# Kernel tuning notes

Hardware: AMD Instinct MI355X
Metric: run time of the kernel (lower is better)

The kernel has to match this reference:

```python
import jax, jax.numpy as jnp
import numpy as np

N = 50000
E = 800000
GENE = 256
H = 128
BN_EPS = 1e-5


def _lin(key, fan_in, fan_out):
    k1, k2 = jax.random.split(key)
    w = jax.random.normal(k1, (fan_in, fan_out), jnp.float32) * (1.0 / np.sqrt(fan_in))
    b = jax.random.normal(k2, (fan_out,), jnp.float32) * 0.01
    return w, b


def setup_inputs() -> dict:
    key = jax.random.key(0)
    ks = jax.random.split(key, 32)
    inp = {}
    inp['x'] = jax.random.normal(ks[0], (N, GENE), jnp.float32)
    inp['edge_index'] = jax.random.randint(ks[1], (2, E), 0, N, jnp.int32)
    dims = [(GENE, H), (H, 2 * H), (2 * H, H), (H, H // 2)]
    ki = 2
    for i, (din, dout) in enumerate(dims, start=1):
        wa, ba = _lin(ks[ki], din, dout); ki += 1
        wb, bb = _lin(ks[ki], dout, dout); ki += 1
        inp[f'w{i}a'], inp[f'b{i}a'] = wa, ba
        inp[f'w{i}b'], inp[f'b{i}b'] = wb, bb
        inp[f'bn{i}_g'] = jnp.ones((dout,), jnp.float32)
        inp[f'bn{i}_b'] = jnp.zeros((dout,), jnp.float32)
        inp[f'bn{i}_m'] = jax.random.normal(ks[ki], (dout,), jnp.float32) * 0.1; ki += 1
        inp[f'bn{i}_v'] = jax.random.uniform(ks[ki], (dout,), jnp.float32, 0.5, 1.5); ki += 1
    wc, bc = _lin(ks[ki], H // 2, 2)
    inp['wc'], inp['bc'] = wc, bc
    return inp


def _gin_layer(h, src, dst, wa, ba, wb, bb, g, be, m, v):
    # GINConv (eps=0): z = x + sum_{j in N(i)} x_j, then 2-layer MLP
    agg = jax.ops.segment_sum(h[src], dst, num_segments=N)
    z = h + agg
    z = jax.nn.relu(z @ wa + ba) @ wb + bb
    # BatchNorm1d (eval: running stats) + ReLU
    z = (z - m) * jax.lax.rsqrt(v + BN_EPS) * g + be
    return jax.nn.relu(z)


def reference(x, edge_index,
              w1a, b1a, w1b, b1b, bn1_g, bn1_b, bn1_m, bn1_v,
              w2a, b2a, w2b, b2b, bn2_g, bn2_b, bn2_m, bn2_v,
              w3a, b3a, w3b, b3b, bn3_g, bn3_b, bn3_m, bn3_v,
              w4a, b4a, w4b, b4b, bn4_g, bn4_b, bn4_m, bn4_v,
              wc, bc):
    src, dst = edge_index[0], edge_index[1]
    h = _gin_layer(x, src, dst, w1a, b1a, w1b, b1b, bn1_g, bn1_b, bn1_m, bn1_v)
    h = _gin_layer(h, src, dst, w2a, b2a, w2b, b2b, bn2_g, bn2_b, bn2_m, bn2_v)
    h = _gin_layer(h, src, dst, w3a, b3a, w3b, b3b, bn3_g, bn3_b, bn3_m, bn3_v)
    h = _gin_layer(h, src, dst, w4a, b4a, w4b, b4b, bn4_g, bn4_b, bn4_m, bn4_v)
    return h @ wc + bc
```

## Files before the change

### kernel.cpp

```cpp
#include <hip/hip_runtime.h>

#define N_NODES 50000
#define N_EDGES 800000
#define BN_EPS 1e-5f
#define K_BUCK 196
#define PART_B 256
#define CHUNK 3125

typedef __attribute__((ext_vector_type(8))) short bshort8;
typedef __attribute__((ext_vector_type(4))) float f32x4;

__device__ inline float bf2f(unsigned int u16) {
    return __uint_as_float(u16 << 16);
}
__device__ inline unsigned short f2bf(float f) {
    unsigned int u = __float_as_uint(f);
    u = (u + 0x7FFFu + ((u >> 16) & 1u)) >> 16;
    return (unsigned short)u;
}


__device__ inline int block_exscan256(int v, int tid, int* total) {
    int lane = tid & 63;
    int wave = tid >> 6;
    int incl = v;
#pragma unroll
    for (int off = 1; off < 64; off <<= 1) {
        int t = __shfl_up(incl, off, 64);
        if (lane >= off) incl += t;
    }
    __shared__ int wsum[4];
    if (lane == 63) wsum[wave] = incl;
    __syncthreads();
    int w0 = wsum[0], w1 = wsum[1], w2 = wsum[2], w3 = wsum[3];
    __syncthreads();
    int wofs = (wave > 0 ? w0 : 0) + (wave > 1 ? w1 : 0) + (wave > 2 ? w2 : 0);
    *total = w0 + w1 + w2 + w3;
    return wofs + incl - v;
}

__global__ __launch_bounds__(256) void scan_reduce_kernel(const int* __restrict__ in,
                                                          int* __restrict__ bsum, int n) {
    int tid = threadIdx.x;
    int i = blockIdx.x * 256 + tid;
    int v = (i < n) ? in[i] : 0;
    int lane = tid & 63;
    int wave = tid >> 6;
#pragma unroll
    for (int off = 32; off > 0; off >>= 1) v += __shfl_down(v, off, 64);
    __shared__ int wsum[4];
    if (lane == 0) wsum[wave] = v;
    __syncthreads();
    if (tid == 0) bsum[blockIdx.x] = wsum[0] + wsum[1] + wsum[2] + wsum[3];
}

__global__ __launch_bounds__(256) void scan_bsum_kernel(int* __restrict__ bsum, int B) {
    int tid = threadIdx.x;
    int v = (tid < B) ? bsum[tid] : 0;
    int total;
    int excl = block_exscan256(v, tid, &total);
    if (tid < B) bsum[tid] = excl;
}

__global__ __launch_bounds__(256) void scan_apply_kernel(const int* __restrict__ in,
                                                         const int* __restrict__ bsum,
                                                         int* __restrict__ out, int n) {
    int tid = threadIdx.x;
    int i = blockIdx.x * 256 + tid;
    int v = (i < n) ? in[i] : 0;
    int total;
    int excl = block_exscan256(v, tid, &total);
    if (i < n) out[i] = bsum[blockIdx.x] + excl;
}


__global__ __launch_bounds__(256) void bucket_count_kernel(const int* __restrict__ dst,
                                                           int* __restrict__ deg,
                                                           int* __restrict__ cnt) {
    __shared__ int lcnt[K_BUCK];
    int tid = threadIdx.x;
    for (int i = tid; i < K_BUCK; i += 256) lcnt[i] = 0;
    __syncthreads();
    int start = blockIdx.x * CHUNK;
    for (int it = tid; it < CHUNK; it += 256) {
        int d = dst[start + it];
        atomicAdd(&lcnt[d >> 8], 1);
        atomicAdd(&deg[d], 1);
    }
    __syncthreads();
    for (int i = tid; i < K_BUCK; i += 256) cnt[i * PART_B + blockIdx.x] = lcnt[i];
}

__global__ __launch_bounds__(256) void partition_kernel(const int* __restrict__ src,
                                                        const int* __restrict__ dst,
                                                        const int* __restrict__ base,
                                                        uint2* __restrict__ P) {
    __shared__ int lofs[K_BUCK];
    int tid = threadIdx.x;
    for (int i = tid; i < K_BUCK; i += 256) lofs[i] = base[i * PART_B + blockIdx.x];
    __syncthreads();
    int start = blockIdx.x * CHUNK;
    for (int it = tid; it < CHUNK; it += 256) {
        int e = start + it;
        int d = dst[e], s = src[e];
        int p = atomicAdd(&lofs[d >> 8], 1);
        P[p] = make_uint2((unsigned)d, (unsigned)s);
    }
}

__global__ __launch_bounds__(256) void fine_scatter_kernel(const uint2* __restrict__ P,
                                                           const int* __restrict__ base,
                                                           const int* __restrict__ deg,
                                                           int* __restrict__ rowptr,
                                                           int* __restrict__ col) {
    __shared__ int wloc[256];
    int b = blockIdx.x;
    int tid = threadIdx.x;
    int nbase = b << 8;
    int nn = min(256, N_NODES - nbase);
    int d = (tid < nn) ? deg[nbase + tid] : 0;
    int total;
    int excl = block_exscan256(d, tid, &total);
    int start = base[b * PART_B];
    int rp = start + excl;
    if (tid < nn) {
        rowptr[nbase + tid] = rp;
        wloc[tid] = rp;
    }
    if (b == K_BUCK - 1 && tid == 0) rowptr[N_NODES] = N_EDGES;
    __syncthreads();
    int end = (b + 1 < K_BUCK) ? base[(b + 1) * PART_B] : N_EDGES;
    for (int e = start + tid; e < end; e += 256) {
        uint2 pr = P[e];
        int rank = atomicAdd(&wloc[pr.x - nbase], 1);
        col[rank] = (int)pr.y;
    }
}


struct WT8 {
    const float* src[8];
    unsigned short* dst[8];
    int K[8];
    int N[8];
};

__global__ __launch_bounds__(256) void wtconv_kernel(WT8 p) {
    int wi = blockIdx.y;
    int K = p.K[wi], N = p.N[wi];
    int idx = blockIdx.x * 256 + threadIdx.x;
    if (idx >= K * N) return;
    int logn = 31 - __clz(N);
    int n = idx & (N - 1);
    int k = idx >> logn;
    p.dst[wi][(size_t)n * K + k] = f2bf(p.src[wi][idx]);
}

__global__ __launch_bounds__(256) void wpconv_kernel(WT8 p) {
    int wi = blockIdx.y;
    int K = p.K[wi], N = p.N[wi];
    int idx = blockIdx.x * 256 + threadIdx.x;
    if (idx >= K * N) return;
    int S = K >> 5;
    int logs = 31 - __clz(S);
    int j = idx & 7;
    int l = (idx >> 3) & 63;
    int rest = idx >> 9;
    int s = rest & (S - 1);
    int t = rest >> logs;
    int k = s * 32 + ((l >> 4) << 3) + j;
    int n = t * 16 + (l & 15);
    p.dst[wi][idx] = f2bf(p.src[wi][(size_t)k * N + n]);
}


__device__ inline void acc8(uint4 v, float* a) {
    a[0] += bf2f(v.x & 0xFFFFu); a[1] += __uint_as_float(v.x & 0xFFFF0000u);
    a[2] += bf2f(v.y & 0xFFFFu); a[3] += __uint_as_float(v.y & 0xFFFF0000u);
    a[4] += bf2f(v.z & 0xFFFFu); a[5] += __uint_as_float(v.z & 0xFFFF0000u);
    a[6] += bf2f(v.w & 0xFFFFu); a[7] += __uint_as_float(v.w & 0xFFFF0000u);
}

template <int BM, int KIN, bool RELU>
__device__ inline void agg_head(const unsigned short* __restrict__ h,
                                const int* __restrict__ rowptr,
                                const int* __restrict__ col,
                                const float* __restrict__ bias,
                                unsigned short* __restrict__ As,
                                int row0, int M, int tid) {
    constexpr int LPN = KIN / 8;
    constexpr int GPS = 256 / LPN;
    constexpr int NSW = BM / GPS;
    constexpr int LDA = KIN + 8;
    const uint4* hv = (const uint4*)h;
    const int l = tid & (LPN - 1);
    const int g = tid / LPN;
#pragma unroll
    for (int sw = 0; sw < NSW; ++sw) {
        int r = sw * GPS + g;
        int node = row0 + r;
        uint4 o = make_uint4(0u, 0u, 0u, 0u);
        if (node < M) {
            float a[8] = {};
            uint4 vs = hv[(size_t)node * LPN + l];
            int s = rowptr[node], epos = rowptr[node + 1];
            int e = s;
            for (; e + 8 <= epos; e += 8) {
                int j0 = col[e],     j1 = col[e + 1], j2 = col[e + 2], j3 = col[e + 3];
                int j4 = col[e + 4], j5 = col[e + 5], j6 = col[e + 6], j7 = col[e + 7];
                uint4 v0 = hv[(size_t)j0 * LPN + l];
                uint4 v1 = hv[(size_t)j1 * LPN + l];
                uint4 v2 = hv[(size_t)j2 * LPN + l];
                uint4 v3 = hv[(size_t)j3 * LPN + l];
                uint4 v4 = hv[(size_t)j4 * LPN + l];
                uint4 v5 = hv[(size_t)j5 * LPN + l];
                uint4 v6 = hv[(size_t)j6 * LPN + l];
                uint4 v7 = hv[(size_t)j7 * LPN + l];
                acc8(v0, a); acc8(v1, a); acc8(v2, a); acc8(v3, a);
                acc8(v4, a); acc8(v5, a); acc8(v6, a); acc8(v7, a);
            }
            if (e + 4 <= epos) {
                int j0 = col[e], j1 = col[e + 1], j2 = col[e + 2], j3 = col[e + 3];
                uint4 v0 = hv[(size_t)j0 * LPN + l];
                uint4 v1 = hv[(size_t)j1 * LPN + l];
                uint4 v2 = hv[(size_t)j2 * LPN + l];
                uint4 v3 = hv[(size_t)j3 * LPN + l];
                acc8(v0, a); acc8(v1, a); acc8(v2, a); acc8(v3, a);
                e += 4;
            }
            if (e + 2 <= epos) {
                int j0 = col[e], j1 = col[e + 1];
                uint4 v0 = hv[(size_t)j0 * LPN + l];
                uint4 v1 = hv[(size_t)j1 * LPN + l];
                acc8(v0, a); acc8(v1, a);
                e += 2;
            }
            if (e < epos) acc8(hv[(size_t)col[e] * LPN + l], a);
            acc8(vs, a);
            if (RELU) {
                float4 b0 = *(const float4*)(bias + l * 8);
                float4 b1 = *(const float4*)(bias + l * 8 + 4);
                a[0] = fmaxf(a[0] + b0.x, 0.f); a[1] = fmaxf(a[1] + b0.y, 0.f);
                a[2] = fmaxf(a[2] + b0.z, 0.f); a[3] = fmaxf(a[3] + b0.w, 0.f);
                a[4] = fmaxf(a[4] + b1.x, 0.f); a[5] = fmaxf(a[5] + b1.y, 0.f);
                a[6] = fmaxf(a[6] + b1.z, 0.f); a[7] = fmaxf(a[7] + b1.w, 0.f);
            }
            o.x = (unsigned int)f2bf(a[0]) | ((unsigned int)f2bf(a[1]) << 16);
            o.y = (unsigned int)f2bf(a[2]) | ((unsigned int)f2bf(a[3]) << 16);
            o.z = (unsigned int)f2bf(a[4]) | ((unsigned int)f2bf(a[5]) << 16);
            o.w = (unsigned int)f2bf(a[6]) | ((unsigned int)f2bf(a[7]) << 16);
        }
        *(uint4*)(&As[r * LDA + l * 8]) = o;
    }
}


__device__ inline void epi_coeff(int mode, int c, const float* bias, const float* g,
                                 const float* be, const float* mu, const float* var,
                                 float* s, float* sh) {
    *s = 1.f; *sh = 0.f;
    if (mode == 0) {
        *sh = bias[c];
    } else if (mode == 1) {
        float t = g[c] * rsqrtf(var[c] + BN_EPS);
        *s = t;
        *sh = be[c] - mu[c] * t + bias[c] * t;
    }
}


template <int NT, bool F32A>
__global__ __launch_bounds__(256) void mfma_gemm2_kernel(
    const void* __restrict__ Ain, const unsigned short* __restrict__ Wt,
    unsigned short* __restrict__ C,
    int M, int K, int Nn, int mode, int gxblocks, int gy) {
    constexpr int BM = 128, BK = 64;
    constexpr int BN = NT * 16;
    constexpr int LDA = BK + 8;
    constexpr int LDB = BK + 8;
    constexpr int LDE = BN + 8;
    constexpr int NB_LD = (BN * BK / 8) / 256;
    __shared__ __align__(16) unsigned short smem[BM * LDA + BN * LDB];
    unsigned short* As = smem;
    unsigned short* Bs = smem + BM * LDA;
    unsigned short* Ep = smem;

    int id = blockIdx.x;
    int lo = id & 7;
    int t = id >> 3;
    int y = t % gy;
    int x = ((t / gy) << 3) | lo;
    if (x >= gxblocks) return;

    const int tid = threadIdx.x;
    const int wv = tid >> 6;
    const int ln = tid & 63;
    const int l15 = ln & 15;
    const int quad = ln >> 4;
    const int row0 = x * BM;
    const int col0 = y * BN;

    const unsigned short* A16 = (const unsigned short*)Ain;
    const float* A32 = (const float*)Ain;

    uint4 Ar[4], Br[NB_LD];

    auto loadA = [&](int k0) {
#pragma unroll
        for (int u = 0; u < 4; ++u) {
            int idx2 = tid + 256 * u;
            int r = idx2 >> 3, cg = (idx2 & 7) * 8;
            int gr = row0 + r;
            if (gr >= M) gr = M - 1;
            if (F32A) {
                float4 f0 = *(const float4*)(A32 + (size_t)gr * K + k0 + cg);
                float4 f1 = *(const float4*)(A32 + (size_t)gr * K + k0 + cg + 4);
                uint4 o;
                o.x = (unsigned)f2bf(f0.x) | ((unsigned)f2bf(f0.y) << 16);
                o.y = (unsigned)f2bf(f0.z) | ((unsigned)f2bf(f0.w) << 16);
                o.z = (unsigned)f2bf(f1.x) | ((unsigned)f2bf(f1.y) << 16);
                o.w = (unsigned)f2bf(f1.z) | ((unsigned)f2bf(f1.w) << 16);
                Ar[u] = o;
            } else {
                Ar[u] = *(const uint4*)(A16 + (size_t)gr * K + k0 + cg);
            }
        }
    };
    auto loadB = [&](int k0) {
#pragma unroll
        for (int u = 0; u < NB_LD; ++u) {
            int idx2 = tid + 256 * u;
            int r = idx2 >> 3, cg = (idx2 & 7) * 8;
            Br[u] = *(const uint4*)(Wt + (size_t)(col0 + r) * K + k0 + cg);
        }
    };
    auto stage = [&]() {
#pragma unroll
        for (int u = 0; u < 4; ++u) {
            int idx2 = tid + 256 * u;
            int r = idx2 >> 3, cg = (idx2 & 7) * 8;
            *(uint4*)(&As[r * LDA + cg]) = Ar[u];
        }
#pragma unroll
        for (int u = 0; u < NB_LD; ++u) {
            int idx2 = tid + 256 * u;
            int r = idx2 >> 3, cg = (idx2 & 7) * 8;
            *(uint4*)(&Bs[r * LDB + cg]) = Br[u];
        }
    };

    f32x4 acc[2][NT] = {};
    const int KT = K >> 6;
    loadA(0);
    loadB(0);
    for (int kt = 0; kt < KT; ++kt) {
        if (kt > 0) __syncthreads();
        stage();
        __syncthreads();
        if (kt + 1 < KT) {
            loadA((kt + 1) * 64);
            loadB((kt + 1) * 64);
        }
#pragma unroll
        for (int kh = 0; kh < 2; ++kh) {
            bshort8 af[2];
#pragma unroll
            for (int mt = 0; mt < 2; ++mt)
                af[mt] = *(const bshort8*)(&As[(wv * 32 + mt * 16 + l15) * LDA + kh * 32 + quad * 8]);
#pragma unroll
            for (int nt = 0; nt < NT; ++nt) {
                bshort8 bf = *(const bshort8*)(&Bs[(nt * 16 + l15) * LDB + kh * 32 + quad * 8]);
                acc[0][nt] = __builtin_amdgcn_mfma_f32_16x16x32_bf16(af[0], bf, acc[0][nt], 0, 0, 0);
                acc[1][nt] = __builtin_amdgcn_mfma_f32_16x16x32_bf16(af[1], bf, acc[1][nt], 0, 0, 0);
            }
        }
    }

    __syncthreads();
#pragma unroll
    for (int nt = 0; nt < NT; ++nt) {
#pragma unroll
        for (int mt = 0; mt < 2; ++mt) {
            int rl = wv * 32 + mt * 16 + quad * 4;
#pragma unroll
            for (int r = 0; r < 4; ++r) {
                float v = acc[mt][nt][r];
                if (mode != 2) v = fmaxf(v, 0.f);
                Ep[(rl + r) * LDE + nt * 16 + l15] = f2bf(v);
            }
        }
    }
    __syncthreads();
    constexpr int CGR = BN / 8;
    constexpr int NU = BM * CGR / 256;
#pragma unroll
    for (int u = 0; u < NU; ++u) {
        int idx2 = tid + 256 * u;
        int r = idx2 / CGR, cg = (idx2 % CGR) * 8;
        int grow = row0 + r;
        if (grow < M)
            *(uint4*)(C + (size_t)grow * Nn + col0 + cg) = *(const uint4*)(&Ep[r * LDE + cg]);
    }
}


template <int KIN, int DH>
__global__ __launch_bounds__(256, 4) void packed_gemm_kernel(
    const unsigned short* __restrict__ A, const unsigned short* __restrict__ Wp,
    int mode, const float* __restrict__ bias, const float* __restrict__ g,
    const float* __restrict__ be, const float* __restrict__ mu, const float* __restrict__ var,
    unsigned short* __restrict__ C, int M) {
    constexpr int BM = 64, BK = 64;
    constexpr int LDA = BK + 8;
    constexpr int LDE = DH + 8;
    constexpr int NT = DH / 64;
    constexpr int KT = KIN / 64;
    constexpr int S = KIN / 32;
    __shared__ __align__(16) unsigned short smem[BM * LDE];
    unsigned short* As = smem;
    unsigned short* Ep = smem;

    const int tid = threadIdx.x;
    const int wv = tid >> 6;
    const int ln = tid & 63;
    const int l15 = ln & 15;
    const int quad = ln >> 4;
    const int tb = wv * NT;
    const int ch = wv * (DH / 4);
    const int row0 = blockIdx.x * BM;

    uint4 Ar[2];
    auto loadA = [&](int k0) {
#pragma unroll
        for (int u = 0; u < 2; ++u) {
            int idx2 = tid + 256 * u;
            int r = idx2 >> 3, cg = (idx2 & 7) * 8;
            int gr = row0 + r;
            if (gr >= M) gr = M - 1;
            Ar[u] = *(const uint4*)(A + (size_t)gr * KIN + k0 + cg);
        }
    };
    auto stageA = [&]() {
#pragma unroll
        for (int u = 0; u < 2; ++u) {
            int idx2 = tid + 256 * u;
            int r = idx2 >> 3, cg = (idx2 & 7) * 8;
            *(uint4*)(&As[r * LDA + cg]) = Ar[u];
        }
    };
    auto loadB = [&](int s, bshort8* d) {
#pragma unroll
        for (int nt = 0; nt < NT; ++nt)
            d[nt] = *(const bshort8*)(Wp + ((size_t)((tb + nt) * S + s) * 64 + ln) * 8);
    };

    f32x4 acc[4][NT] = {};
    bshort8 bf[NT], bnx[NT];
    loadA(0);
    loadB(0, bf);
    for (int kt = 0; kt < KT; ++kt) {
        if (kt > 0) __syncthreads();
        stageA();
        __syncthreads();
        if (kt + 1 < KT) loadA((kt + 1) * 64);
#pragma unroll
        for (int kh = 0; kh < 2; ++kh) {
            int st = kt * 2 + kh;
            if (st + 1 < S) loadB(st + 1, bnx);
            bshort8 af[4];
#pragma unroll
            for (int mt = 0; mt < 4; ++mt)
                af[mt] = *(const bshort8*)(&As[(mt * 16 + l15) * LDA + kh * 32 + quad * 8]);
#pragma unroll
            for (int nt = 0; nt < NT; ++nt)
#pragma unroll
                for (int mt = 0; mt < 4; ++mt)
                    acc[mt][nt] = __builtin_amdgcn_mfma_f32_16x16x32_bf16(af[mt], bf[nt], acc[mt][nt], 0, 0, 0);
            if (st + 1 < S) {
#pragma unroll
                for (int nt = 0; nt < NT; ++nt) bf[nt] = bnx[nt];
            }
        }
    }
    __syncthreads();
#pragma unroll
    for (int nt = 0; nt < NT; ++nt) {
        int c = ch + nt * 16 + l15;
        float s, sh;
        epi_coeff(mode, c, bias, g, be, mu, var, &s, &sh);
#pragma unroll
        for (int mt = 0; mt < 4; ++mt) {
            int rl = mt * 16 + quad * 4;
#pragma unroll
            for (int r = 0; r < 4; ++r) {
                float v = acc[mt][nt][r] * s + sh;
                if (mode != 2) v = fmaxf(v, 0.f);
                Ep[(rl + r) * LDE + c] = f2bf(v);
            }
        }
    }
    __syncthreads();
    constexpr int CGR = DH / 8;
    constexpr int NU = BM * CGR / 256;
#pragma unroll
    for (int u = 0; u < NU; ++u) {
        int idx2 = tid + 256 * u;
        int r = idx2 / CGR, cg = (idx2 % CGR) * 8;
        int grow = row0 + r;
        if (grow < M)
            *(uint4*)(C + (size_t)grow * DH + cg) = *(const uint4*)(&Ep[r * LDE + cg]);
    }
}


template <int BM, int KIN, int DH, bool ARELU>
__global__ __launch_bounds__(256, 4) void agg_gemm_kernel(
    const unsigned short* __restrict__ h, const int* __restrict__ rowptr,
    const int* __restrict__ col, const float* __restrict__ abias,
    const unsigned short* __restrict__ Wp,
    int mode, const float* __restrict__ bias, const float* __restrict__ g,
    const float* __restrict__ be, const float* __restrict__ mu, const float* __restrict__ var,
    unsigned short* __restrict__ C, int M) {
    constexpr int MT = BM / 16;
    constexpr int LDA = KIN + 8;
    constexpr int LDE = DH + 8;
    constexpr int NT = DH / 64;
    constexpr int S = KIN / 32;
    constexpr int LMX = (LDA > LDE) ? LDA : LDE;
    __shared__ __align__(16) unsigned short smem[BM * LMX];
    unsigned short* As = smem;
    unsigned short* Ep = smem;

    const int tid = threadIdx.x;
    const int wv = tid >> 6;
    const int ln = tid & 63;
    const int l15 = ln & 15;
    const int quad = ln >> 4;
    const int tb = wv * NT;
    const int ch = wv * (DH / 4);
    const int row0 = blockIdx.x * BM;

    auto loadB = [&](int s, bshort8* d) {
#pragma unroll
        for (int nt = 0; nt < NT; ++nt)
            d[nt] = *(const bshort8*)(Wp + ((size_t)((tb + nt) * S + s) * 64 + ln) * 8);
    };

    bshort8 bf[NT], bnx[NT];
    loadB(0, bf);
    agg_head<BM, KIN, ARELU>(h, rowptr, col, abias, As, row0, M, tid);
    __syncthreads();

    f32x4 acc[MT][NT] = {};
#pragma unroll
    for (int ks = 0; ks < S; ++ks) {
        if (ks + 1 < S) loadB(ks + 1, bnx);
        bshort8 af[MT];
#pragma unroll
        for (int mt = 0; mt < MT; ++mt)
            af[mt] = *(const bshort8*)(&As[(mt * 16 + l15) * LDA + (ks >> 1) * 64 + (ks & 1) * 32 + quad * 8]);
#pragma unroll
        for (int nt = 0; nt < NT; ++nt)
#pragma unroll
            for (int mt = 0; mt < MT; ++mt)
                acc[mt][nt] = __builtin_amdgcn_mfma_f32_16x16x32_bf16(af[mt], bf[nt], acc[mt][nt], 0, 0, 0);
        if (ks + 1 < S) {
#pragma unroll
            for (int nt = 0; nt < NT; ++nt) bf[nt] = bnx[nt];
        }
    }
    __syncthreads();
#pragma unroll
    for (int nt = 0; nt < NT; ++nt) {
        int c = ch + nt * 16 + l15;
        float s, sh;
        epi_coeff(mode, c, bias, g, be, mu, var, &s, &sh);
#pragma unroll
        for (int mt = 0; mt < MT; ++mt) {
            int rl = mt * 16 + quad * 4;
#pragma unroll
            for (int r = 0; r < 4; ++r) {
                float v = acc[mt][nt][r] * s + sh;
                if (mode != 2) v = fmaxf(v, 0.f);
                Ep[(rl + r) * LDE + c] = f2bf(v);
            }
        }
    }
    __syncthreads();
    constexpr int CGR = DH / 8;
    constexpr int NU = BM * CGR / 256;
#pragma unroll
    for (int u = 0; u < NU; ++u) {
        int idx2 = tid + 256 * u;
        int r = idx2 / CGR, cg = (idx2 % CGR) * 8;
        int grow = row0 + r;
        if (grow < M)
            *(uint4*)(C + (size_t)grow * DH + cg) = *(const uint4*)(&Ep[r * LDE + cg]);
    }
}


template <int BM, int KIN, int DH1, int DH2, bool ARELU>
__global__ __launch_bounds__(256, 4) void agg_mlp_kernel(
    const unsigned short* __restrict__ h, const int* __restrict__ rowptr,
    const int* __restrict__ col, const float* __restrict__ abias,
    const unsigned short* __restrict__ Wp1, const unsigned short* __restrict__ Wp2,
    int mode1, const float* __restrict__ b1, const float* __restrict__ g1,
    const float* __restrict__ be1, const float* __restrict__ mu1, const float* __restrict__ var1,
    int mode2, const float* __restrict__ b2, const float* __restrict__ g2,
    const float* __restrict__ be2, const float* __restrict__ mu2, const float* __restrict__ var2,
    unsigned short* __restrict__ C, int M) {
    constexpr int MT = BM / 16;
    constexpr int LDA = KIN + 8;
    constexpr int LT1 = DH1 + 8;
    constexpr int LDE = DH2 + 8;
    constexpr int NT1 = DH1 / 64;
    constexpr int NT2 = DH2 / 64;
    constexpr int S1 = KIN / 32;
    constexpr int S2 = DH1 / 32;
    constexpr int LM0 = (LDA > LT1) ? LDA : LT1;
    constexpr int LMX = (LM0 > LDE) ? LM0 : LDE;
    __shared__ __align__(16) unsigned short smem[BM * LMX];
    unsigned short* As = smem;
    unsigned short* T1 = smem;

    const int tid = threadIdx.x;
    const int wv = tid >> 6;
    const int ln = tid & 63;
    const int l15 = ln & 15;
    const int quad = ln >> 4;
    const int tb1 = wv * NT1;
    const int tb2 = wv * NT2;
    const int ch1 = wv * (DH1 / 4);
    const int ch2 = wv * (DH2 / 4);
    const int row0 = blockIdx.x * BM;

    auto loadB1 = [&](int s, bshort8* d) {
#pragma unroll
        for (int nt = 0; nt < NT1; ++nt)
            d[nt] = *(const bshort8*)(Wp1 + ((size_t)((tb1 + nt) * S1 + s) * 64 + ln) * 8);
    };
    auto loadB2 = [&](int s, bshort8* d) {
#pragma unroll
        for (int nt = 0; nt < NT2; ++nt)
            d[nt] = *(const bshort8*)(Wp2 + ((size_t)((tb2 + nt) * S2 + s) * 64 + ln) * 8);
    };

    bshort8 bf[NT1], bnx[NT1], bf2[NT2];
    loadB1(0, bf);
    agg_head<BM, KIN, ARELU>(h, rowptr, col, abias, As, row0, M, tid);
    __syncthreads();

    f32x4 acc1[MT][NT1] = {};
#pragma unroll
    for (int ks = 0; ks < S1; ++ks) {
        if (ks + 1 < S1) loadB1(ks + 1, bnx);
        bshort8 af[MT];
#pragma unroll
        for (int mt = 0; mt < MT; ++mt)
            af[mt] = *(const bshort8*)(&As[(mt * 16 + l15) * LDA + (ks >> 1) * 64 + (ks & 1) * 32 + quad * 8]);
#pragma unroll
        for (int nt = 0; nt < NT1; ++nt)
#pragma unroll
            for (int mt = 0; mt < MT; ++mt)
                acc1[mt][nt] = __builtin_amdgcn_mfma_f32_16x16x32_bf16(af[mt], bf[nt], acc1[mt][nt], 0, 0, 0);
        if (ks + 1 < S1) {
#pragma unroll
            for (int nt = 0; nt < NT1; ++nt) bf[nt] = bnx[nt];
        }
    }
    __syncthreads();
#pragma unroll
    for (int nt = 0; nt < NT1; ++nt) {
        int c = ch1 + nt * 16 + l15;
        float s, sh;
        epi_coeff(mode1, c, b1, g1, be1, mu1, var1, &s, &sh);
#pragma unroll
        for (int mt = 0; mt < MT; ++mt) {
            int rl = mt * 16 + quad * 4;
#pragma unroll
            for (int r = 0; r < 4; ++r) {
                float v = acc1[mt][nt][r] * s + sh;
                if (mode1 != 2) v = fmaxf(v, 0.f);
                T1[(rl + r) * LT1 + c] = f2bf(v);
            }
        }
    }
    loadB2(0, bf2);
    __syncthreads();

    f32x4 acc2[MT][NT2] = {};
    bshort8 bnx2[NT2];
#pragma unroll
    for (int ks = 0; ks < S2; ++ks) {
        if (ks + 1 < S2) loadB2(ks + 1, bnx2);
        bshort8 af[MT];
#pragma unroll
        for (int mt = 0; mt < MT; ++mt)
            af[mt] = *(const bshort8*)(&T1[(mt * 16 + l15) * LT1 + ks * 32 + quad * 8]);
#pragma unroll
        for (int nt = 0; nt < NT2; ++nt)
#pragma unroll
            for (int mt = 0; mt < MT; ++mt)
                acc2[mt][nt] = __builtin_amdgcn_mfma_f32_16x16x32_bf16(af[mt], bf2[nt], acc2[mt][nt], 0, 0, 0);
        if (ks + 1 < S2) {
#pragma unroll
            for (int nt = 0; nt < NT2; ++nt) bf2[nt] = bnx2[nt];
        }
    }
    __syncthreads();

    unsigned short* Ep = T1;
#pragma unroll
    for (int nt = 0; nt < NT2; ++nt) {
        int c = ch2 + nt * 16 + l15;
        float s, sh;
        epi_coeff(mode2, c, b2, g2, be2, mu2, var2, &s, &sh);
#pragma unroll
        for (int mt = 0; mt < MT; ++mt) {
            int rl = mt * 16 + quad * 4;
#pragma unroll
            for (int r = 0; r < 4; ++r) {
                float v = acc2[mt][nt][r] * s + sh;
                if (mode2 != 2) v = fmaxf(v, 0.f);
                Ep[(rl + r) * LDE + c] = f2bf(v);
            }
        }
    }
    __syncthreads();
    constexpr int CGR = DH2 / 8;
    constexpr int NU = BM * CGR / 256;
#pragma unroll
    for (int u = 0; u < NU; ++u) {
        int idx2 = tid + 256 * u;
        int r = idx2 / CGR, cg = (idx2 % CGR) * 8;
        int grow = row0 + r;
        if (grow < M)
            *(uint4*)(C + (size_t)grow * DH2 + cg) = *(const uint4*)(&Ep[r * LDE + cg]);
    }
}


__global__ __launch_bounds__(256, 4) void agg_cls_kernel(
    const unsigned short* __restrict__ h, const int* __restrict__ rowptr,
    const int* __restrict__ col, const float* __restrict__ abias,
    const unsigned short* __restrict__ Wp,
    const float* __restrict__ bias, const float* __restrict__ g,
    const float* __restrict__ be, const float* __restrict__ mu, const float* __restrict__ var,
    const float* __restrict__ wcls, const float* __restrict__ bcls,
    float* __restrict__ outp, int M) {
    constexpr int BM = 64, KIN = 64, DH = 64;
    constexpr int LDA = KIN + 8;
    constexpr int LDE = DH + 8;
    constexpr int NT = 1;
    constexpr int S = KIN / 32;
    __shared__ __align__(16) unsigned short smem[BM * LDA];
    unsigned short* As = smem;
    unsigned short* Ep = smem;

    const int tid = threadIdx.x;
    const int wv = tid >> 6;
    const int ln = tid & 63;
    const int l15 = ln & 15;
    const int quad = ln >> 4;
    const int tb = wv;
    const int ch = wv * 16;
    const int row0 = blockIdx.x * BM;

    auto loadB = [&](int s, bshort8* d) {
        d[0] = *(const bshort8*)(Wp + ((size_t)(tb * S + s) * 64 + ln) * 8);
    };

    bshort8 bf[NT], bnx[NT];
    loadB(0, bf);
    agg_head<BM, KIN, true>(h, rowptr, col, abias, As, row0, M, tid);
    __syncthreads();

    f32x4 acc[4][NT] = {};
#pragma unroll
    for (int ks = 0; ks < S; ++ks) {
        if (ks + 1 < S) loadB(ks + 1, bnx);
        bshort8 af[4];
#pragma unroll
        for (int mt = 0; mt < 4; ++mt)
            af[mt] = *(const bshort8*)(&As[(mt * 16 + l15) * LDA + ks * 32 + quad * 8]);
#pragma unroll
        for (int mt = 0; mt < 4; ++mt)
            acc[mt][0] = __builtin_amdgcn_mfma_f32_16x16x32_bf16(af[mt], bf[0], acc[mt][0], 0, 0, 0);
        if (ks + 1 < S) bf[0] = bnx[0];
    }
    __syncthreads();
    {
        int c = ch + l15;
        float s, sh;
        epi_coeff(1, c, bias, g, be, mu, var, &s, &sh);
#pragma unroll
        for (int mt = 0; mt < 4; ++mt) {
            int rl = mt * 16 + quad * 4;
#pragma unroll
            for (int r = 0; r < 4; ++r) {
                float v = fmaxf(acc[mt][0][r] * s + sh, 0.f);
                Ep[(rl + r) * LDE + c] = f2bf(v);
            }
        }
    }
    __syncthreads();
    if (tid < 128) {
        int r = tid >> 1, j = tid & 1;
        int grow = row0 + r;
        if (grow < M) {
            float s = 0.f;
#pragma unroll 8
            for (int k = 0; k < 64; ++k)
                s += bf2f(Ep[r * LDE + k]) * wcls[k * 2 + j];
            outp[(size_t)grow * 2 + j] = s + bcls[j];
        }
    }
}


extern "C" void kernel_launch(void* const* d_in, const int* in_sizes, int n_in,
                              void* d_out, int out_size, void* d_ws, size_t ws_size,
                              hipStream_t stream) {
    const float* x = (const float*)d_in[0];
    const int* ei = (const int*)d_in[1];
    const int* src = ei;
    const int* dst = ei + N_EDGES;
    const float* w[4][2];
    const float* b[4][2];
    const float* bng[4];
    const float* bnb[4];
    const float* bnm[4];
    const float* bnv[4];
    int idx = 2;
    for (int i = 0; i < 4; ++i) {
        w[i][0] = (const float*)d_in[idx++];
        b[i][0] = (const float*)d_in[idx++];
        w[i][1] = (const float*)d_in[idx++];
        b[i][1] = (const float*)d_in[idx++];
        bng[i] = (const float*)d_in[idx++];
        bnb[i] = (const float*)d_in[idx++];
        bnm[i] = (const float*)d_in[idx++];
        bnv[i] = (const float*)d_in[idx++];
    }
    const float* wc = (const float*)d_in[idx++];
    const float* bc = (const float*)d_in[idx++];
    float* out = (float*)d_out;

    char* ws = (char*)d_ws;
    size_t off = 0;
    auto alloc = [&](size_t bytes) {
        char* p = ws + off;
        off = (off + bytes + 255) & ~(size_t)255;
        return p;
    };
    int* deg = (int*)alloc((size_t)N_NODES * 4);
    int* rowptr = (int*)alloc((size_t)(N_NODES + 1) * 4);
    int* cnt = (int*)alloc((size_t)K_BUCK * PART_B * 4);
    int* bsum2 = (int*)alloc((size_t)K_BUCK * 4);
    int* col = (int*)alloc((size_t)N_EDGES * 4 + 64);
    uint2* P = (uint2*)alloc((size_t)N_EDGES * 8);
    unsigned short* bufA = (unsigned short*)alloc((size_t)N_NODES * 256 * 2);
    unsigned short* bufB = (unsigned short*)alloc((size_t)N_NODES * 256 * 2);
    unsigned short* bufC = (unsigned short*)alloc((size_t)N_NODES * 256 * 2);
    const int dims_in[4] = {256, 128, 256, 128};
    const int dims_h[4] = {128, 256, 128, 64};
    unsigned short* wt[4][2];
    unsigned short* wp[4][2];
    for (int L = 0; L < 4; ++L) {
        wt[L][0] = (unsigned short*)alloc((size_t)dims_in[L] * dims_h[L] * 2);
        wt[L][1] = (unsigned short*)alloc((size_t)dims_h[L] * dims_h[L] * 2);
        wp[L][0] = (unsigned short*)alloc((size_t)dims_in[L] * dims_h[L] * 2);
        wp[L][1] = (unsigned short*)alloc((size_t)dims_h[L] * dims_h[L] * 2);
    }
    (void)ws_size;

    WT8 p;
    for (int L = 0; L < 4; ++L) {
        p.src[L * 2] = w[L][0];     p.dst[L * 2] = wt[L][0];
        p.K[L * 2] = dims_in[L];    p.N[L * 2] = dims_h[L];
        p.src[L * 2 + 1] = w[L][1]; p.dst[L * 2 + 1] = wt[L][1];
        p.K[L * 2 + 1] = dims_h[L]; p.N[L * 2 + 1] = dims_h[L];
    }
    wtconv_kernel<<<dim3(256, 8), 256, 0, stream>>>(p);
    WT8 q = p;
    for (int L = 0; L < 4; ++L) {
        q.dst[L * 2] = wp[L][0];
        q.dst[L * 2 + 1] = wp[L][1];
    }
    wpconv_kernel<<<dim3(256, 8), 256, 0, stream>>>(q);

    hipMemsetAsync(deg, 0, (size_t)N_NODES * 4, stream);
    bucket_count_kernel<<<PART_B, 256, 0, stream>>>(dst, deg, cnt);
    scan_reduce_kernel<<<K_BUCK, 256, 0, stream>>>(cnt, bsum2, K_BUCK * PART_B);
    scan_bsum_kernel<<<1, 256, 0, stream>>>(bsum2, K_BUCK);
    scan_apply_kernel<<<K_BUCK, 256, 0, stream>>>(cnt, bsum2, cnt, K_BUCK * PART_B);
    partition_kernel<<<PART_B, 256, 0, stream>>>(src, dst, cnt, P);
    fine_scatter_kernel<<<K_BUCK, 256, 0, stream>>>(P, cnt, deg, rowptr, col);

    const int gx = (N_NODES + 127) / 128;
    const int gxp = ((gx + 7) / 8) * 8;
    const int gx32 = (N_NODES + 31) / 32;
    const int gx64 = (N_NODES + 63) / 64;
    const int M = N_NODES;

    mfma_gemm2_kernel<8, true><<<gxp, 256, 0, stream>>>(
        x, wt[0][0], bufA, M, 256, 128, 2, gx, 1);

    agg_gemm_kernel<64, 128, 128, true><<<gx64, 256, 0, stream>>>(
        bufA, rowptr, col, b[0][0], wp[0][1],
        1, b[0][1], bng[0], bnb[0], bnm[0], bnv[0], bufC, M);

    agg_mlp_kernel<32, 128, 256, 256, false><<<gx32, 256, 0, stream>>>(
        bufC, rowptr, col, nullptr, wp[1][0], wp[1][1],
        0, b[1][0], nullptr, nullptr, nullptr, nullptr,
        1, b[1][1], bng[1], bnb[1], bnm[1], bnv[1],
        bufA, M);

    packed_gemm_kernel<256, 128><<<gx64, 256, 0, stream>>>(
        bufA, wp[2][0], 2, nullptr, nullptr, nullptr, nullptr, nullptr, bufB, M);

    agg_mlp_kernel<64, 128, 128, 64, true><<<gx64, 256, 0, stream>>>(
        bufB, rowptr, col, b[2][0], wp[2][1], wp[3][0],
        1, b[2][1], bng[2], bnb[2], bnm[2], bnv[2],
        2, nullptr, nullptr, nullptr, nullptr, nullptr,
        bufC, M);

    agg_cls_kernel<<<gx64, 256, 0, stream>>>(
        bufC, rowptr, col, b[3][0], wp[3][1],
        b[3][1], bng[3], bnb[3], bnm[3], bnv[3], wc, bc, out, M);
}
```

Before: 392.5 us.

## Fuse layer-3 pre-projection GEMM into layer-2 aggregation MLP kernel

Adds a three-stage agg_mlp3 kernel that, after layer 2's aggregation and two MLP GEMMs with BN, applies layer 3's first weight (linear, no bias) in shared memory before writing out. This removes the separate packed_gemm launch and the write/read round trip of the 256-wide layer-2 output through global memory, writing only a 128-wide tensor instead. In exchange, the fused kernel holds more register state and more sequential stages per block at BM=32, which may lower occupancy. The A-fragment indexing is also simplified to ks*32, which gives the same offsets as before.

```diff
diff --git a/kernel.cpp b/kernel.cpp
--- a/kernel.cpp
+++ b/kernel.cpp
@@ -404,115 +404,6 @@
 }
 
 
-template <int KIN, int DH>
-__global__ __launch_bounds__(256, 4) void packed_gemm_kernel(
-    const unsigned short* __restrict__ A, const unsigned short* __restrict__ Wp,
-    int mode, const float* __restrict__ bias, const float* __restrict__ g,
-    const float* __restrict__ be, const float* __restrict__ mu, const float* __restrict__ var,
-    unsigned short* __restrict__ C, int M) {
-    constexpr int BM = 64, BK = 64;
-    constexpr int LDA = BK + 8;
-    constexpr int LDE = DH + 8;
-    constexpr int NT = DH / 64;
-    constexpr int KT = KIN / 64;
-    constexpr int S = KIN / 32;
-    __shared__ __align__(16) unsigned short smem[BM * LDE];
-    unsigned short* As = smem;
-    unsigned short* Ep = smem;
-
-    const int tid = threadIdx.x;
-    const int wv = tid >> 6;
-    const int ln = tid & 63;
-    const int l15 = ln & 15;
-    const int quad = ln >> 4;
-    const int tb = wv * NT;
-    const int ch = wv * (DH / 4);
-    const int row0 = blockIdx.x * BM;
-
-    uint4 Ar[2];
-    auto loadA = [&](int k0) {
-#pragma unroll
-        for (int u = 0; u < 2; ++u) {
-            int idx2 = tid + 256 * u;
-            int r = idx2 >> 3, cg = (idx2 & 7) * 8;
-            int gr = row0 + r;
-            if (gr >= M) gr = M - 1;
-            Ar[u] = *(const uint4*)(A + (size_t)gr * KIN + k0 + cg);
-        }
-    };
-    auto stageA = [&]() {
-#pragma unroll
-        for (int u = 0; u < 2; ++u) {
-            int idx2 = tid + 256 * u;
-            int r = idx2 >> 3, cg = (idx2 & 7) * 8;
-            *(uint4*)(&As[r * LDA + cg]) = Ar[u];
-        }
-    };
-    auto loadB = [&](int s, bshort8* d) {
-#pragma unroll
-        for (int nt = 0; nt < NT; ++nt)
-            d[nt] = *(const bshort8*)(Wp + ((size_t)((tb + nt) * S + s) * 64 + ln) * 8);
-    };
-
-    f32x4 acc[4][NT] = {};
-    bshort8 bf[NT], bnx[NT];
-    loadA(0);
-    loadB(0, bf);
-    for (int kt = 0; kt < KT; ++kt) {
-        if (kt > 0) __syncthreads();
-        stageA();
-        __syncthreads();
-        if (kt + 1 < KT) loadA((kt + 1) * 64);
-#pragma unroll
-        for (int kh = 0; kh < 2; ++kh) {
-            int st = kt * 2 + kh;
-            if (st + 1 < S) loadB(st + 1, bnx);
-            bshort8 af[4];
-#pragma unroll
-            for (int mt = 0; mt < 4; ++mt)
-                af[mt] = *(const bshort8*)(&As[(mt * 16 + l15) * LDA + kh * 32 + quad * 8]);
-#pragma unroll
-            for (int nt = 0; nt < NT; ++nt)
-#pragma unroll
-                for (int mt = 0; mt < 4; ++mt)
-                    acc[mt][nt] = __builtin_amdgcn_mfma_f32_16x16x32_bf16(af[mt], bf[nt], acc[mt][nt], 0, 0, 0);
-            if (st + 1 < S) {
-#pragma unroll
-                for (int nt = 0; nt < NT; ++nt) bf[nt] = bnx[nt];
-            }
-        }
-    }
-    __syncthreads();
-#pragma unroll
-    for (int nt = 0; nt < NT; ++nt) {
-        int c = ch + nt * 16 + l15;
-        float s, sh;
-        epi_coeff(mode, c, bias, g, be, mu, var, &s, &sh);
-#pragma unroll
-        for (int mt = 0; mt < 4; ++mt) {
-            int rl = mt * 16 + quad * 4;
-#pragma unroll
-            for (int r = 0; r < 4; ++r) {
-                float v = acc[mt][nt][r] * s + sh;
-                if (mode != 2) v = fmaxf(v, 0.f);
-                Ep[(rl + r) * LDE + c] = f2bf(v);
-            }
-        }
-    }
-    __syncthreads();
-    constexpr int CGR = DH / 8;
-    constexpr int NU = BM * CGR / 256;
-#pragma unroll
-    for (int u = 0; u < NU; ++u) {
-        int idx2 = tid + 256 * u;
-        int r = idx2 / CGR, cg = (idx2 % CGR) * 8;
-        int grow = row0 + r;
-        if (grow < M)
-            *(uint4*)(C + (size_t)grow * DH + cg) = *(const uint4*)(&Ep[r * LDE + cg]);
-    }
-}
-
-
 template <int BM, int KIN, int DH, bool ARELU>
 __global__ __launch_bounds__(256, 4) void agg_gemm_kernel(
     const unsigned short* __restrict__ h, const int* __restrict__ rowptr,
@@ -558,7 +449,7 @@
         bshort8 af[MT];
 #pragma unroll
         for (int mt = 0; mt < MT; ++mt)
-            af[mt] = *(const bshort8*)(&As[(mt * 16 + l15) * LDA + (ks >> 1) * 64 + (ks & 1) * 32 + quad * 8]);
+            af[mt] = *(const bshort8*)(&As[(mt * 16 + l15) * LDA + ks * 32 + quad * 8]);
 #pragma unroll
         for (int nt = 0; nt < NT; ++nt)
 #pragma unroll
@@ -658,7 +549,7 @@
         bshort8 af[MT];
 #pragma unroll
         for (int mt = 0; mt < MT; ++mt)
-            af[mt] = *(const bshort8*)(&As[(mt * 16 + l15) * LDA + (ks >> 1) * 64 + (ks & 1) * 32 + quad * 8]);
+            af[mt] = *(const bshort8*)(&As[(mt * 16 + l15) * LDA + ks * 32 + quad * 8]);
 #pragma unroll
         for (int nt = 0; nt < NT1; ++nt)
 #pragma unroll
@@ -737,6 +628,194 @@
         int grow = row0 + r;
         if (grow < M)
             *(uint4*)(C + (size_t)grow * DH2 + cg) = *(const uint4*)(&Ep[r * LDE + cg]);
+    }
+}
+
+
+template <int BM, int KIN, int DH1, int DH2, int DH3, bool ARELU>
+__global__ __launch_bounds__(256, 4) void agg_mlp3_kernel(
+    const unsigned short* __restrict__ h, const int* __restrict__ rowptr,
+    const int* __restrict__ col, const float* __restrict__ abias,
+    const unsigned short* __restrict__ Wp1, const unsigned short* __restrict__ Wp2,
+    const unsigned short* __restrict__ Wp3,
+    int mode1, const float* __restrict__ b1, const float* __restrict__ g1,
+    const float* __restrict__ be1, const float* __restrict__ mu1, const float* __restrict__ var1,
+    int mode2, const float* __restrict__ b2, const float* __restrict__ g2,
+    const float* __restrict__ be2, const float* __restrict__ mu2, const float* __restrict__ var2,
+    unsigned short* __restrict__ C, int M) {
+    constexpr int MT = BM / 16;
+    constexpr int LDA = KIN + 8;
+    constexpr int LT1 = DH1 + 8;
+    constexpr int LT2 = DH2 + 8;
+    constexpr int LDE = DH3 + 8;
+    constexpr int NT1 = DH1 / 64;
+    constexpr int NT2 = DH2 / 64;
+    constexpr int NT3 = DH3 / 64;
+    constexpr int S1 = KIN / 32;
+    constexpr int S2 = DH1 / 32;
+    constexpr int S3 = DH2 / 32;
+    constexpr int LM0 = (LDA > LT1) ? LDA : LT1;
+    constexpr int LM1 = (LM0 > LT2) ? LM0 : LT2;
+    constexpr int LMX = (LM1 > LDE) ? LM1 : LDE;
+    __shared__ __align__(16) unsigned short smem[BM * LMX];
+    unsigned short* As = smem;
+    unsigned short* T1 = smem;
+    unsigned short* T2 = smem;
+
+    const int tid = threadIdx.x;
+    const int wv = tid >> 6;
+    const int ln = tid & 63;
+    const int l15 = ln & 15;
+    const int quad = ln >> 4;
+    const int tb1 = wv * NT1;
+    const int tb2 = wv * NT2;
+    const int tb3 = wv * NT3;
+    const int ch1 = wv * (DH1 / 4);
+    const int ch2 = wv * (DH2 / 4);
+    const int ch3 = wv * (DH3 / 4);
+    const int row0 = blockIdx.x * BM;
+
+    auto loadB1 = [&](int s, bshort8* d) {
+#pragma unroll
+        for (int nt = 0; nt < NT1; ++nt)
+            d[nt] = *(const bshort8*)(Wp1 + ((size_t)((tb1 + nt) * S1 + s) * 64 + ln) * 8);
+    };
+    auto loadB2 = [&](int s, bshort8* d) {
+#pragma unroll
+        for (int nt = 0; nt < NT2; ++nt)
+            d[nt] = *(const bshort8*)(Wp2 + ((size_t)((tb2 + nt) * S2 + s) * 64 + ln) * 8);
+    };
+    auto loadB3 = [&](int s, bshort8* d) {
+#pragma unroll
+        for (int nt = 0; nt < NT3; ++nt)
+            d[nt] = *(const bshort8*)(Wp3 + ((size_t)((tb3 + nt) * S3 + s) * 64 + ln) * 8);
+    };
+
+    bshort8 bf[NT1], bnx[NT1];
+    loadB1(0, bf);
+    agg_head<BM, KIN, ARELU>(h, rowptr, col, abias, As, row0, M, tid);
+    __syncthreads();
+
+    f32x4 acc1[MT][NT1] = {};
+#pragma unroll
+    for (int ks = 0; ks < S1; ++ks) {
+        if (ks + 1 < S1) loadB1(ks + 1, bnx);
+        bshort8 af[MT];
+#pragma unroll
+        for (int mt = 0; mt < MT; ++mt)
+            af[mt] = *(const bshort8*)(&As[(mt * 16 + l15) * LDA + ks * 32 + quad * 8]);
+#pragma unroll
+        for (int nt = 0; nt < NT1; ++nt)
+#pragma unroll
+            for (int mt = 0; mt < MT; ++mt)
+                acc1[mt][nt] = __builtin_amdgcn_mfma_f32_16x16x32_bf16(af[mt], bf[nt], acc1[mt][nt], 0, 0, 0);
+        if (ks + 1 < S1) {
+#pragma unroll
+            for (int nt = 0; nt < NT1; ++nt) bf[nt] = bnx[nt];
+        }
+    }
+    __syncthreads();
+#pragma unroll
+    for (int nt = 0; nt < NT1; ++nt) {
+        int c = ch1 + nt * 16 + l15;
+        float s, sh;
+        epi_coeff(mode1, c, b1, g1, be1, mu1, var1, &s, &sh);
+#pragma unroll
+        for (int mt = 0; mt < MT; ++mt) {
+            int rl = mt * 16 + quad * 4;
+#pragma unroll
+            for (int r = 0; r < 4; ++r) {
+                float v = acc1[mt][nt][r] * s + sh;
+                if (mode1 != 2) v = fmaxf(v, 0.f);
+                T1[(rl + r) * LT1 + c] = f2bf(v);
+            }
+        }
+    }
+    bshort8 bf2[NT2], bnx2[NT2];
+    loadB2(0, bf2);
+    __syncthreads();
+
+    f32x4 acc2[MT][NT2] = {};
+#pragma unroll
+    for (int ks = 0; ks < S2; ++ks) {
+        if (ks + 1 < S2) loadB2(ks + 1, bnx2);
+        bshort8 af[MT];
+#pragma unroll
+        for (int mt = 0; mt < MT; ++mt)
+            af[mt] = *(const bshort8*)(&T1[(mt * 16 + l15) * LT1 + ks * 32 + quad * 8]);
+#pragma unroll
+        for (int nt = 0; nt < NT2; ++nt)
+#pragma unroll
+            for (int mt = 0; mt < MT; ++mt)
+                acc2[mt][nt] = __builtin_amdgcn_mfma_f32_16x16x32_bf16(af[mt], bf2[nt], acc2[mt][nt], 0, 0, 0);
+        if (ks + 1 < S2) {
+#pragma unroll
+            for (int nt = 0; nt < NT2; ++nt) bf2[nt] = bnx2[nt];
+        }
+    }
+    __syncthreads();
+#pragma unroll
+    for (int nt = 0; nt < NT2; ++nt) {
+        int c = ch2 + nt * 16 + l15;
+        float s, sh;
+        epi_coeff(mode2, c, b2, g2, be2, mu2, var2, &s, &sh);
+#pragma unroll
+        for (int mt = 0; mt < MT; ++mt) {
+            int rl = mt * 16 + quad * 4;
+#pragma unroll
+            for (int r = 0; r < 4; ++r) {
+                float v = acc2[mt][nt][r] * s + sh;
+                if (mode2 != 2) v = fmaxf(v, 0.f);
+                T2[(rl + r) * LT2 + c] = f2bf(v);
+            }
+        }
+    }
+    bshort8 bf3[NT3], bnx3[NT3];
+    loadB3(0, bf3);
+    __syncthreads();
+
+    f32x4 acc3[MT][NT3] = {};
+#pragma unroll
+    for (int ks = 0; ks < S3; ++ks) {
+        if (ks + 1 < S3) loadB3(ks + 1, bnx3);
+        bshort8 af[MT];
+#pragma unroll
+        for (int mt = 0; mt < MT; ++mt)
+            af[mt] = *(const bshort8*)(&T2[(mt * 16 + l15) * LT2 + ks * 32 + quad * 8]);
+#pragma unroll
+        for (int nt = 0; nt < NT3; ++nt)
+#pragma unroll
+            for (int mt = 0; mt < MT; ++mt)
+                acc3[mt][nt] = __builtin_amdgcn_mfma_f32_16x16x32_bf16(af[mt], bf3[nt], acc3[mt][nt], 0, 0, 0);
+        if (ks + 1 < S3) {
+#pragma unroll
+            for (int nt = 0; nt < NT3; ++nt) bf3[nt] = bnx3[nt];
+        }
+    }
+    __syncthreads();
+
+    unsigned short* Ep = smem;
+#pragma unroll
+    for (int nt = 0; nt < NT3; ++nt) {
+        int c = ch3 + nt * 16 + l15;
+#pragma unroll
+        for (int mt = 0; mt < MT; ++mt) {
+            int rl = mt * 16 + quad * 4;
+#pragma unroll
+            for (int r = 0; r < 4; ++r)
+                Ep[(rl + r) * LDE + c] = f2bf(acc3[mt][nt][r]);
+        }
+    }
+    __syncthreads();
+    constexpr int CGR = DH3 / 8;
+    constexpr int NU = BM * CGR / 256;
+#pragma unroll
+    for (int u = 0; u < NU; ++u) {
+        int idx2 = tid + 256 * u;
+        int r = idx2 / CGR, cg = (idx2 % CGR) * 8;
+        int grow = row0 + r;
+        if (grow < M)
+            *(uint4*)(C + (size_t)grow * DH3 + cg) = *(const uint4*)(&Ep[r * LDE + cg]);
     }
 }
 
@@ -911,22 +990,19 @@
         bufA, rowptr, col, b[0][0], wp[0][1],
         1, b[0][1], bng[0], bnb[0], bnm[0], bnv[0], bufC, M);
 
-    agg_mlp_kernel<32, 128, 256, 256, false><<<gx32, 256, 0, stream>>>(
-        bufC, rowptr, col, nullptr, wp[1][0], wp[1][1],
+    agg_mlp3_kernel<32, 128, 256, 256, 128, false><<<gx32, 256, 0, stream>>>(
+        bufC, rowptr, col, nullptr, wp[1][0], wp[1][1], wp[2][0],
         0, b[1][0], nullptr, nullptr, nullptr, nullptr,
         1, b[1][1], bng[1], bnb[1], bnm[1], bnv[1],
         bufA, M);
 
-    packed_gemm_kernel<256, 128><<<gx64, 256, 0, stream>>>(
-        bufA, wp[2][0], 2, nullptr, nullptr, nullptr, nullptr, nullptr, bufB, M);
-
     agg_mlp_kernel<64, 128, 128, 64, true><<<gx64, 256, 0, stream>>>(
-        bufB, rowptr, col, b[2][0], wp[2][1], wp[3][0],
+        bufA, rowptr, col, b[2][0], wp[2][1], wp[3][0],
         1, b[2][1], bng[2], bnb[2], bnm[2], bnv[2],
         2, nullptr, nullptr, nullptr, nullptr, nullptr,
-        bufC, M);
+        bufB, M);
 
     agg_cls_kernel<<<gx64, 256, 0, stream>>>(
-        bufC, rowptr, col, b[3][0], wp[3][1],
+        bufB, rowptr, col, b[3][0], wp[3][1],
         b[3][1], bng[3], bnb[3], bnm[3], bnv[3], wc, bc, out, M);
 }
```

After: 381.4 us, median of 2. 2.8% less time.
